# Kernel tuning notes

Measured on AMD Instinct MI355X. Metric: run time of the kernel, lower is better.

The kernel has to match this reference:

```python
import jax, jax.numpy as jnp
import numpy as np

TOP_K = 2
TEMPERATURE = 2.0


def setup_inputs() -> dict:
    key = jax.random.key(0)
    k1, k2, k3 = jax.random.split(key, 3)
    x = jax.random.normal(k1, (16384, 2048), dtype=jnp.float32)
    gate_w = jax.random.normal(k2, (64, 2048), dtype=jnp.float32) * 0.02
    gate_b = jax.random.normal(k3, (64,), dtype=jnp.float32) * 0.02
    expert_maturity = jnp.ones((64,), dtype=jnp.int32)  # all mature -> top-k branch
    return {"x": x, "gate_w": gate_w, "gate_b": gate_b, "expert_maturity": expert_maturity}


def _routing(logits, expert_maturity):
    # branch 1: any immature expert -> temperature softmax over all experts
    def soft_branch(lg):
        return jax.nn.softmax(lg / TEMPERATURE, axis=-1)

    # branch 2: all mature -> top-k selection, softmax over selected, scatter into zeros
    def topk_branch(lg):
        top_w, top_idx = jax.lax.top_k(lg, TOP_K)          # [N, K]
        top_sm = jax.nn.softmax(top_w, axis=-1)            # [N, K]
        n = lg.shape[0]
        rows = jnp.arange(n)[:, None]                      # [N, 1]
        return jnp.zeros_like(lg).at[rows, top_idx].set(top_sm)

    any_immature = jnp.any(expert_maturity == 0)
    return jax.lax.cond(any_immature, soft_branch, topk_branch, logits)


def reference(x, gate_w, gate_b, expert_maturity):
    # logits = x @ W^T + b : [N, E]
    logits = jnp.einsum("nd,ed->ne", x, gate_w) + gate_b
    return _routing(logits, expert_maturity)
```

## Files before the change

### kernel.cpp

```cpp
#include <hip/hip_runtime.h>
#include <math.h>


#define NROWS 16384
#define DIM   2048
#define NEXP  64
#define BM    16
#define TPB   256
#define KSLICE 512
#define KSTEPS (KSLICE / 32)

typedef __attribute__((ext_vector_type(4))) float f32x4;
typedef __attribute__((ext_vector_type(8))) short bf16x8;

__global__ void wfrag_kernel(const float* __restrict__ gw,
                             unsigned short* __restrict__ wsH,
                             unsigned short* __restrict__ wsL) {
  int slot  = blockIdx.x * 256 + threadIdx.x;
  int lane  = slot & 63;
  int t     = (slot >> 6) & 3;
  int kstep = slot >> 8;
  int e  = 16 * t + (lane & 15);
  int k0 = kstep * 32 + (lane >> 4) * 8;
  const float* src = gw + (size_t)e * DIM + k0;
  bf16x8 vh, vl;
#pragma unroll
  for (int j = 0; j < 8; ++j) {
    float w = src[j];
    unsigned u = __float_as_uint(w);
    vh[j] = (short)(u >> 16);
    float hi = __uint_as_float(u & 0xffff0000u);
    float rl = w - hi;
    vl[j] = (short)(__float_as_uint(rl) >> 16);
  }
  ((bf16x8*)wsH)[slot] = vh;
  ((bf16x8*)wsL)[slot] = vl;
}

__global__ __launch_bounds__(TPB, 4)
void router_mfma(const float* __restrict__ x,
                 const unsigned short* __restrict__ wsH,
                 const unsigned short* __restrict__ wsL,
                 const float* __restrict__ gb,
                 const int* __restrict__ mat,
                 float* __restrict__ out) {
  __shared__ float slab[4 * BM * NEXP];
  __shared__ float p_a[BM], p_b[BM];
  __shared__ int   p_i[BM], p_j[BM];
  __shared__ int   s_flag;

  const int tid  = threadIdx.x;
  const int ksl  = tid >> 6;
  const int lane = tid & 63;
  const int m    = lane & 15;
  const int kg   = lane >> 4;
  const int row0 = blockIdx.x * BM;

  if (tid < 64) {
    unsigned long long b = __ballot(mat[lane] == 0);
    if (lane == 0) s_flag = (b != 0ull) ? 1 : 0;
  }

  f32x4 acc[4];
#pragma unroll
  for (int t = 0; t < 4; ++t) acc[t] = (f32x4)0.0f;

  const size_t bbase = (size_t)((ksl * KSTEPS * 4) * 64 + lane);
  const bf16x8* bHp = (const bf16x8*)wsH + bbase;
  const bf16x8* bLp = (const bf16x8*)wsL + bbase;

  const float* xb = x + (size_t)(row0 + m) * DIM + ksl * KSLICE + kg * 8;

  float4 xr[4][2];
#pragma unroll
  for (int p = 0; p < 4; ++p) {
    xr[p][0] = *(const float4*)(xb + p * 32);
    xr[p][1] = *(const float4*)(xb + p * 32 + 4);
  }

#pragma unroll 4
  for (int s = 0; s < KSTEPS; ++s) {
    const int slot = s & 3;
    bf16x8 ah, al;
#pragma unroll
    for (int q = 0; q < 2; ++q) {
      float4 v = xr[slot][q];
      float ff[4] = {v.x, v.y, v.z, v.w};
#pragma unroll
      for (int j = 0; j < 4; ++j) {
        unsigned u = __float_as_uint(ff[j]);
        ah[q * 4 + j] = (short)(u >> 16);
        float hi = __uint_as_float(u & 0xffff0000u);
        float rl = ff[j] - hi;
        al[q * 4 + j] = (short)(__float_as_uint(rl) >> 16);
      }
    }
    {
      const int sp = (s + 4 < KSTEPS) ? (s + 4) : s;
      xr[slot][0] = *(const float4*)(xb + sp * 32);
      xr[slot][1] = *(const float4*)(xb + sp * 32 + 4);
    }
    bf16x8 bh[4], bl[4];
#pragma unroll
    for (int t = 0; t < 4; ++t) {
      bh[t] = bHp[(size_t)s * 256 + t * 64];
      bl[t] = bLp[(size_t)s * 256 + t * 64];
    }
#pragma unroll
    for (int t = 0; t < 4; ++t) {
      acc[t] = __builtin_amdgcn_mfma_f32_16x16x32_bf16(ah, bh[t], acc[t], 0, 0, 0);
      acc[t] = __builtin_amdgcn_mfma_f32_16x16x32_bf16(ah, bl[t], acc[t], 0, 0, 0);
      acc[t] = __builtin_amdgcn_mfma_f32_16x16x32_bf16(al, bh[t], acc[t], 0, 0, 0);
    }
  }

  {
    float* sl = slab + ksl * (BM * NEXP);
#pragma unroll
    for (int t = 0; t < 4; ++t)
#pragma unroll
      for (int reg = 0; reg < 4; ++reg)
        sl[(kg * 4 + reg) * NEXP + 16 * t + m] = acc[t][reg];
  }
  __syncthreads();

  for (int idx = tid; idx < BM * NEXP; idx += TPB) {
    float v = slab[idx] + slab[1024 + idx] + slab[2048 + idx] + slab[3072 + idx]
            + gb[idx & (NEXP - 1)];
    slab[idx] = v;
  }
  __syncthreads();

  const int flag = s_flag;

  if (tid < BM) {
    const float* rowp = slab + tid * NEXP;
    if (flag == 0) {
      float m1 = -1e30f, m2 = -1e30f;
      int i1 = 0, i2 = 0;
      for (int ee = 0; ee < NEXP; ++ee) {
        int e = (ee + tid) & (NEXP - 1);
        float v = rowp[e];
        if (v > m1) { m2 = m1; i2 = i1; m1 = v; i1 = e; }
        else if (v > m2) { m2 = v; i2 = e; }
      }
      float t = expf(m2 - m1);
      float pa = 1.0f / (1.0f + t);
      p_a[tid] = pa;
      p_b[tid] = t * pa;
      p_i[tid] = i1;
      p_j[tid] = i2;
    } else {
      float mx = -1e30f;
      for (int ee = 0; ee < NEXP; ++ee)
        mx = fmaxf(mx, rowp[(ee + tid) & (NEXP - 1)]);
      float ssum = 0.0f;
      for (int ee = 0; ee < NEXP; ++ee)
        ssum += expf((rowp[(ee + tid) & (NEXP - 1)] - mx) * 0.5f);
      p_a[tid] = mx;
      p_b[tid] = 1.0f / ssum;
    }
  }
  __syncthreads();

  {
    int q  = tid;
    int r  = q >> 4;
    int e0 = (q & 15) * 4;
    float4 v;
    if (flag == 0) {
      int i1 = p_i[r], i2 = p_j[r];
      float a = p_a[r], b = p_b[r];
      v.x = (e0 + 0 == i1) ? a : (e0 + 0 == i2) ? b : 0.0f;
      v.y = (e0 + 1 == i1) ? a : (e0 + 1 == i2) ? b : 0.0f;
      v.z = (e0 + 2 == i1) ? a : (e0 + 2 == i2) ? b : 0.0f;
      v.w = (e0 + 3 == i1) ? a : (e0 + 3 == i2) ? b : 0.0f;
    } else {
      float mx = p_a[r], inv = p_b[r];
      const float* rowp = slab + r * NEXP + e0;
      v.x = expf((rowp[0] - mx) * 0.5f) * inv;
      v.y = expf((rowp[1] - mx) * 0.5f) * inv;
      v.z = expf((rowp[2] - mx) * 0.5f) * inv;
      v.w = expf((rowp[3] - mx) * 0.5f) * inv;
    }
    *(float4*)(out + (size_t)(row0 + r) * NEXP + e0) = v;
  }
}

extern "C" void kernel_launch(void* const* d_in, const int* in_sizes, int n_in,
                              void* d_out, int out_size, void* d_ws, size_t ws_size,
                              hipStream_t stream) {
  const float* x  = (const float*)d_in[0];
  const float* gw = (const float*)d_in[1];
  const float* gb = (const float*)d_in[2];
  const int*   mt = (const int*)d_in[3];
  float* outp = (float*)d_out;
  (void)in_sizes; (void)n_in; (void)out_size; (void)ws_size;

  unsigned short* wsH = (unsigned short*)d_ws;
  unsigned short* wsL = wsH + 64 * DIM;

  wfrag_kernel<<<64, 256, 0, stream>>>(gw, wsH, wsL);
  router_mfma<<<NROWS / BM, TPB, 0, stream>>>(x, wsH, wsL, gb, mt, outp);
}
```

Measured before the change: 221.6 us.

## Stage gate weights in double-buffered LDS and give each wave its own rows

Each block now covers 64 rows instead of 16, with each of the 4 waves owning 16 rows over the full K dimension, so the split-K reduction through shared memory is gone. The bf16 hi/lo weight fragments are loaded cooperatively into a double-buffered LDS ring one chunk ahead and shared by all waves, which cuts repeated L2 reads of the weights. Each wave prefetches its x chunk one step ahead, and the bias is added during the accumulator store. In exchange the grid shrinks to 256 blocks with launch bounds of 1 block per CU, so fewer waves are available to hide global-load latency on the x stream.

```diff
diff --git a/kernel.cpp b/kernel.cpp
--- a/kernel.cpp
+++ b/kernel.cpp
@@ -5,10 +5,10 @@
 #define NROWS 16384
 #define DIM   2048
 #define NEXP  64
-#define BM    16
+#define BM    64
 #define TPB   256
-#define KSLICE 512
-#define KSTEPS (KSLICE / 32)
+#define CH    4
+#define NCH   (DIM / 32 / CH)
 
 typedef __attribute__((ext_vector_type(4))) float f32x4;
 typedef __attribute__((ext_vector_type(8))) short bf16x8;
@@ -37,20 +37,20 @@
   ((bf16x8*)wsL)[slot] = vl;
 }
 
-__global__ __launch_bounds__(TPB, 4)
+__global__ __launch_bounds__(TPB, 1)
 void router_mfma(const float* __restrict__ x,
                  const unsigned short* __restrict__ wsH,
                  const unsigned short* __restrict__ wsL,
                  const float* __restrict__ gb,
                  const int* __restrict__ mat,
                  float* __restrict__ out) {
-  __shared__ float slab[4 * BM * NEXP];
+  __shared__ __align__(16) char lds[2 * CH * 8 * 1024];
   __shared__ float p_a[BM], p_b[BM];
   __shared__ int   p_i[BM], p_j[BM];
   __shared__ int   s_flag;
 
   const int tid  = threadIdx.x;
-  const int ksl  = tid >> 6;
+  const int wave = tid >> 6;
   const int lane = tid & 63;
   const int m    = lane & 15;
   const int kg   = lane >> 4;
@@ -65,69 +65,100 @@
 #pragma unroll
   for (int t = 0; t < 4; ++t) acc[t] = (f32x4)0.0f;
 
-  const size_t bbase = (size_t)((ksl * KSTEPS * 4) * 64 + lane);
-  const bf16x8* bHp = (const bf16x8*)wsH + bbase;
-  const bf16x8* bLp = (const bf16x8*)wsL + bbase;
-
-  const float* xb = x + (size_t)(row0 + m) * DIM + ksl * KSLICE + kg * 8;
-
-  float4 xr[4][2];
-#pragma unroll
-  for (int p = 0; p < 4; ++p) {
-    xr[p][0] = *(const float4*)(xb + p * 32);
-    xr[p][1] = *(const float4*)(xb + p * 32 + 4);
-  }
-
-#pragma unroll 4
-  for (int s = 0; s < KSTEPS; ++s) {
-    const int slot = s & 3;
-    bf16x8 ah, al;
-#pragma unroll
-    for (int q = 0; q < 2; ++q) {
-      float4 v = xr[slot][q];
-      float ff[4] = {v.x, v.y, v.z, v.w};
-#pragma unroll
-      for (int j = 0; j < 4; ++j) {
-        unsigned u = __float_as_uint(ff[j]);
-        ah[q * 4 + j] = (short)(u >> 16);
-        float hi = __uint_as_float(u & 0xffff0000u);
-        float rl = ff[j] - hi;
-        al[q * 4 + j] = (short)(__float_as_uint(rl) >> 16);
-      }
-    }
-    {
-      const int sp = (s + 4 < KSTEPS) ? (s + 4) : s;
-      xr[slot][0] = *(const float4*)(xb + sp * 32);
-      xr[slot][1] = *(const float4*)(xb + sp * 32 + 4);
-    }
-    bf16x8 bh[4], bl[4];
-#pragma unroll
-    for (int t = 0; t < 4; ++t) {
-      bh[t] = bHp[(size_t)s * 256 + t * 64];
-      bl[t] = bLp[(size_t)s * 256 + t * 64];
-    }
-#pragma unroll
-    for (int t = 0; t < 4; ++t) {
-      acc[t] = __builtin_amdgcn_mfma_f32_16x16x32_bf16(ah, bh[t], acc[t], 0, 0, 0);
-      acc[t] = __builtin_amdgcn_mfma_f32_16x16x32_bf16(ah, bl[t], acc[t], 0, 0, 0);
-      acc[t] = __builtin_amdgcn_mfma_f32_16x16x32_bf16(al, bh[t], acc[t], 0, 0, 0);
-    }
-  }
-
+  const bf16x8* wsHf = (const bf16x8*)wsH;
+  const bf16x8* wsLf = (const bf16x8*)wsL;
+
+  bf16x8 breg[8];
+  const float* xb = x + (size_t)(row0 + 16 * wave + m) * DIM + kg * 8;
+
+#pragma unroll
+  for (int u = 0; u < 8; ++u) {
+    int t = u >> 1;
+    size_t slot = (size_t)((0 * CH + wave) * 4 + t);
+    breg[u] = (u & 1) ? wsLf[slot * 64 + lane] : wsHf[slot * 64 + lane];
+  }
+  float4 xc[CH][2], xn[CH][2];
+#pragma unroll
+  for (int st = 0; st < CH; ++st) {
+    xc[st][0] = *(const float4*)(xb + st * 32);
+    xc[st][1] = *(const float4*)(xb + st * 32 + 4);
+  }
+#pragma unroll
+  for (int u = 0; u < 8; ++u)
+    *(bf16x8*)(lds + (wave * 8 + u) * 1024 + lane * 16) = breg[u];
+  __syncthreads();
+
+#pragma unroll 1
+  for (int c = 0; c < NCH; ++c) {
+    const int par = (c & 1) * 32768;
+    const bool more = (c + 1 < NCH);
+    if (more) {
+#pragma unroll
+      for (int u = 0; u < 8; ++u) {
+        int t = u >> 1;
+        size_t slot = (size_t)(((c + 1) * CH + wave) * 4 + t);
+        breg[u] = (u & 1) ? wsLf[slot * 64 + lane] : wsHf[slot * 64 + lane];
+      }
+      const float* xp = xb + (c + 1) * (CH * 32);
+#pragma unroll
+      for (int st = 0; st < CH; ++st) {
+        xn[st][0] = *(const float4*)(xp + st * 32);
+        xn[st][1] = *(const float4*)(xp + st * 32 + 4);
+      }
+    }
+#pragma unroll
+    for (int st = 0; st < CH; ++st) {
+      bf16x8 bh[4], bl[4];
+#pragma unroll
+      for (int t = 0; t < 4; ++t) {
+        bh[t] = *(const bf16x8*)(lds + par + (st * 8 + 2 * t) * 1024 + lane * 16);
+        bl[t] = *(const bf16x8*)(lds + par + (st * 8 + 2 * t + 1) * 1024 + lane * 16);
+      }
+      bf16x8 ah, al;
+#pragma unroll
+      for (int q = 0; q < 2; ++q) {
+        float4 v = xc[st][q];
+        float ff[4] = {v.x, v.y, v.z, v.w};
+#pragma unroll
+        for (int j = 0; j < 4; ++j) {
+          unsigned u = __float_as_uint(ff[j]);
+          ah[q * 4 + j] = (short)(u >> 16);
+          float hi = __uint_as_float(u & 0xffff0000u);
+          float rl = ff[j] - hi;
+          al[q * 4 + j] = (short)(__float_as_uint(rl) >> 16);
+        }
+      }
+#pragma unroll
+      for (int t = 0; t < 4; ++t) {
+        acc[t] = __builtin_amdgcn_mfma_f32_16x16x32_bf16(ah, bh[t], acc[t], 0, 0, 0);
+        acc[t] = __builtin_amdgcn_mfma_f32_16x16x32_bf16(ah, bl[t], acc[t], 0, 0, 0);
+        acc[t] = __builtin_amdgcn_mfma_f32_16x16x32_bf16(al, bh[t], acc[t], 0, 0, 0);
+      }
+    }
+    if (more) {
+      const int par2 = ((c + 1) & 1) * 32768;
+#pragma unroll
+      for (int u = 0; u < 8; ++u)
+        *(bf16x8*)(lds + par2 + (wave * 8 + u) * 1024 + lane * 16) = breg[u];
+#pragma unroll
+      for (int st = 0; st < CH; ++st) {
+        xc[st][0] = xn[st][0];
+        xc[st][1] = xn[st][1];
+      }
+    }
+    __syncthreads();
+  }
+
+  float* slab = (float*)lds;
   {
-    float* sl = slab + ksl * (BM * NEXP);
+    float gbv[4];
+#pragma unroll
+    for (int t = 0; t < 4; ++t) gbv[t] = gb[16 * t + m];
 #pragma unroll
     for (int t = 0; t < 4; ++t)
 #pragma unroll
       for (int reg = 0; reg < 4; ++reg)
-        sl[(kg * 4 + reg) * NEXP + 16 * t + m] = acc[t][reg];
-  }
-  __syncthreads();
-
-  for (int idx = tid; idx < BM * NEXP; idx += TPB) {
-    float v = slab[idx] + slab[1024 + idx] + slab[2048 + idx] + slab[3072 + idx]
-            + gb[idx & (NEXP - 1)];
-    slab[idx] = v;
+        slab[(16 * wave + kg * 4 + reg) * NEXP + 16 * t + m] = acc[t][reg] + gbv[t];
   }
   __syncthreads();
 
@@ -163,8 +194,9 @@
   }
   __syncthreads();
 
-  {
-    int q  = tid;
+#pragma unroll
+  for (int i = 0; i < 4; ++i) {
+    int q  = tid + i * TPB;
     int r  = q >> 4;
     int e0 = (q & 15) * 4;
     float4 v;
```

Result: faster. 206.9 us (-6.6%).

## Stage x through LDS with async DMA double buffering and prefetch weights

Applied to the files above, without the earlier changes.

The x tile is now loaded with asynchronous global-to-LDS DMA into a per-wave double buffer, in chunks of four k-steps. Explicit vmcnt waits overlap the next chunk's load with the MFMA work on the current one. The weight fragments are software-prefetched one k-step ahead in registers. The aim is to hide global-memory latency, but the 64KB LDS stage and launch bounds lowered to 2 reduce occupancy, and the hand-written waitcnt ordering carries a correctness risk.

```diff
diff --git a/kernel.cpp b/kernel.cpp
--- a/kernel.cpp
+++ b/kernel.cpp
@@ -8,10 +8,18 @@
 #define BM    16
 #define TPB   256
 #define KSLICE 512
-#define KSTEPS (KSLICE / 32)
+#define KSTEPS 16
+#define CH    4
+#define NCH   (KSTEPS / CH)
 
 typedef __attribute__((ext_vector_type(4))) float f32x4;
 typedef __attribute__((ext_vector_type(8))) short bf16x8;
+
+__device__ inline void dma16(const void* g, void* l) {
+  __builtin_amdgcn_global_load_lds(
+      (const __attribute__((address_space(1))) unsigned int*)g,
+      (__attribute__((address_space(3))) unsigned int*)l, 16, 0, 0);
+}
 
 __global__ void wfrag_kernel(const float* __restrict__ gw,
                              unsigned short* __restrict__ wsH,
@@ -37,14 +45,14 @@
   ((bf16x8*)wsL)[slot] = vl;
 }
 
-__global__ __launch_bounds__(TPB, 4)
+__global__ __launch_bounds__(TPB, 2)
 void router_mfma(const float* __restrict__ x,
                  const unsigned short* __restrict__ wsH,
                  const unsigned short* __restrict__ wsL,
                  const float* __restrict__ gb,
                  const int* __restrict__ mat,
                  float* __restrict__ out) {
-  __shared__ float slab[4 * BM * NEXP];
+  __shared__ __align__(16) float xstage[4 * 2 * BM * CH * 32];
   __shared__ float p_a[BM], p_b[BM];
   __shared__ int   p_i[BM], p_j[BM];
   __shared__ int   s_flag;
@@ -65,55 +73,75 @@
 #pragma unroll
   for (int t = 0; t < 4; ++t) acc[t] = (f32x4)0.0f;
 
-  const size_t bbase = (size_t)((ksl * KSTEPS * 4) * 64 + lane);
-  const bf16x8* bHp = (const bf16x8*)wsH + bbase;
-  const bf16x8* bLp = (const bf16x8*)wsL + bbase;
-
-  const float* xb = x + (size_t)(row0 + m) * DIM + ksl * KSLICE + kg * 8;
-
-  float4 xr[4][2];
-#pragma unroll
-  for (int p = 0; p < 4; ++p) {
-    xr[p][0] = *(const float4*)(xb + p * 32);
-    xr[p][1] = *(const float4*)(xb + p * 32 + 4);
-  }
-
-#pragma unroll 4
-  for (int s = 0; s < KSTEPS; ++s) {
-    const int slot = s & 3;
-    bf16x8 ah, al;
-#pragma unroll
-    for (int q = 0; q < 2; ++q) {
-      float4 v = xr[slot][q];
-      float ff[4] = {v.x, v.y, v.z, v.w};
-#pragma unroll
-      for (int j = 0; j < 4; ++j) {
-        unsigned u = __float_as_uint(ff[j]);
-        ah[q * 4 + j] = (short)(u >> 16);
-        float hi = __uint_as_float(u & 0xffff0000u);
-        float rl = ff[j] - hi;
-        al[q * 4 + j] = (short)(__float_as_uint(rl) >> 16);
-      }
-    }
-    {
-      const int sp = (s + 4 < KSTEPS) ? (s + 4) : s;
-      xr[slot][0] = *(const float4*)(xb + sp * 32);
-      xr[slot][1] = *(const float4*)(xb + sp * 32 + 4);
-    }
-    bf16x8 bh[4], bl[4];
-#pragma unroll
-    for (int t = 0; t < 4; ++t) {
-      bh[t] = bHp[(size_t)s * 256 + t * 64];
-      bl[t] = bLp[(size_t)s * 256 + t * 64];
-    }
-#pragma unroll
-    for (int t = 0; t < 4; ++t) {
-      acc[t] = __builtin_amdgcn_mfma_f32_16x16x32_bf16(ah, bh[t], acc[t], 0, 0, 0);
-      acc[t] = __builtin_amdgcn_mfma_f32_16x16x32_bf16(ah, bl[t], acc[t], 0, 0, 0);
-      acc[t] = __builtin_amdgcn_mfma_f32_16x16x32_bf16(al, bh[t], acc[t], 0, 0, 0);
-    }
-  }
-
+  const bf16x8* wsHf = (const bf16x8*)wsH;
+  const bf16x8* wsLf = (const bf16x8*)wsL;
+  const int gs0 = ksl * KSTEPS;
+
+  const float* xg = x + (size_t)(row0 + (lane >> 5)) * DIM + ksl * KSLICE + (lane & 31) * 4;
+  float* xbuf = xstage + ksl * (2 * BM * CH * 32);
+
+#pragma unroll
+  for (int i = 0; i < 8; ++i)
+    dma16(xg + (size_t)(2 * i) * DIM, xbuf + i * 256);
+  asm volatile("s_waitcnt vmcnt(0)" ::: "memory");
+
+  bf16x8 bh[4], bl[4];
+#pragma unroll
+  for (int t = 0; t < 4; ++t) {
+    bh[t] = wsHf[(size_t)((gs0 + 0) * 4 + t) * 64 + lane];
+    bl[t] = wsLf[(size_t)((gs0 + 0) * 4 + t) * 64 + lane];
+  }
+
+#pragma unroll 1
+  for (int c = 0; c < NCH; ++c) {
+    if (c + 1 < NCH) {
+      float* dst = xbuf + ((c + 1) & 1) * 2048;
+      const float* src = xg + (c + 1) * (CH * 32);
+#pragma unroll
+      for (int i = 0; i < 8; ++i)
+        dma16(src + (size_t)(2 * i) * DIM, dst + i * 256);
+    }
+    asm volatile("s_waitcnt vmcnt(16)" ::: "memory");
+    const float* xc = xbuf + (c & 1) * 2048;
+
+#pragma unroll
+    for (int st = 0; st < CH; ++st) {
+      const int gs  = c * CH + st;
+      const int gsn = (gs + 1 < KSTEPS) ? (gs + 1) : gs;
+      bf16x8 bhn[4], bln[4];
+#pragma unroll
+      for (int t = 0; t < 4; ++t) {
+        bhn[t] = wsHf[(size_t)((gs0 + gsn) * 4 + t) * 64 + lane];
+        bln[t] = wsLf[(size_t)((gs0 + gsn) * 4 + t) * 64 + lane];
+      }
+      const float* xr = xc + m * 128 + st * 32 + kg * 8;
+      float4 v0 = *(const float4*)xr;
+      float4 v1 = *(const float4*)(xr + 4);
+      bf16x8 ah, al;
+      {
+        float ff[8] = {v0.x, v0.y, v0.z, v0.w, v1.x, v1.y, v1.z, v1.w};
+#pragma unroll
+        for (int j = 0; j < 8; ++j) {
+          unsigned u = __float_as_uint(ff[j]);
+          ah[j] = (short)(u >> 16);
+          float hi = __uint_as_float(u & 0xffff0000u);
+          float rl = ff[j] - hi;
+          al[j] = (short)(__float_as_uint(rl) >> 16);
+        }
+      }
+#pragma unroll
+      for (int t = 0; t < 4; ++t) {
+        acc[t] = __builtin_amdgcn_mfma_f32_16x16x32_bf16(ah, bh[t], acc[t], 0, 0, 0);
+        acc[t] = __builtin_amdgcn_mfma_f32_16x16x32_bf16(ah, bl[t], acc[t], 0, 0, 0);
+        acc[t] = __builtin_amdgcn_mfma_f32_16x16x32_bf16(al, bh[t], acc[t], 0, 0, 0);
+      }
+#pragma unroll
+      for (int t = 0; t < 4; ++t) { bh[t] = bhn[t]; bl[t] = bln[t]; }
+    }
+  }
+
+  __syncthreads();
+  float* slab = xstage;
   {
     float* sl = slab + ksl * (BM * NEXP);
 #pragma unroll
```

Result: faster. 216.5 us (-2.3%).
